# Optimization experiments

Hardware: AMD Instinct MI355X
Metric: run time of the kernel (lower is better)

Reference implementation:

```python
import jax, jax.numpy as jnp
import numpy as np

RES = (256, 256, 256)
CH = 16
RR = 8  # ceil(log2(256))
N_PTS = 262144


def grid_sample_2d(plane, gx, gy):
    """Bilinear grid_sample, align_corners=True.
    plane: (C, H, W); gx in [-1,1] indexes W, gy indexes H. Returns (N, C)."""
    C, H, W = plane.shape
    ix = (gx + 1.0) * 0.5 * (W - 1)
    iy = (gy + 1.0) * 0.5 * (H - 1)
    x0f = jnp.floor(ix)
    y0f = jnp.floor(iy)
    wx = ix - x0f
    wy = iy - y0f
    x0 = jnp.clip(x0f.astype(jnp.int32), 0, W - 1)
    x1 = jnp.clip(x0 + 1, 0, W - 1)
    y0 = jnp.clip(y0f.astype(jnp.int32), 0, H - 1)
    y1 = jnp.clip(y0 + 1, 0, H - 1)
    v00 = plane[:, y0, x0]  # (C, N)
    v01 = plane[:, y0, x1]
    v10 = plane[:, y1, x0]
    v11 = plane[:, y1, x1]
    out = (v00 * (1 - wx) * (1 - wy) + v01 * wx * (1 - wy)
           + v10 * (1 - wx) * wy + v11 * wx * wy)
    return out.T  # (N, C)


def integrate(P, coords):
    """P: (N, 2*CH, RR) with real part channels [:CH], imag [CH:].
    coords: (N,) in [-1,1]. Fourier-basis numerical integration (real part)."""
    c = (coords + 1.0) * 0.5 * (2 ** RR - 1)  # (N,)
    coef = jnp.concatenate([jnp.zeros((1,), jnp.float32),
                            2.0 ** jnp.arange(RR - 1, dtype=jnp.float32)]) / (2 ** RR)
    theta = 2.0 * jnp.pi * c[:, None] * coef  # (N, RR)
    # Re(exp(i*theta) . P_complex) = cos.Re(P) - sin.Im(P)
    re = jnp.einsum('nr,ncr->nc', jnp.cos(theta), P[:, :CH, :])
    im = jnp.einsum('nr,ncr->nc', jnp.sin(theta), P[:, CH:, :])
    return re - im  # (N, CH)


def setup_inputs() -> dict:
    key = jax.random.key(0)
    k0, k1, k2, k3 = jax.random.split(key, 4)
    inputs = jax.random.uniform(k0, (N_PTS, 3), dtype=jnp.float32,
                                minval=-1.0, maxval=1.0)
    C = 2 * RR * CH
    Pu = 0.001 * jax.random.normal(k1, (1, C, RES[1], RES[2]), dtype=jnp.float32)
    Pv = 0.001 * jax.random.normal(k2, (1, C, RES[0], RES[2]), dtype=jnp.float32)
    Pw = 0.001 * jax.random.normal(k3, (1, C, RES[0], RES[1]), dtype=jnp.float32)
    return {"inputs": inputs, "Pu": Pu, "Pv": Pv, "Pw": Pw}


def reference(inputs, Pu, Pv, Pw):
    c0, c1, c2 = inputs[:, 0], inputs[:, 1], inputs[:, 2]
    # grid last-dim (x,y): x indexes width (last plane axis), y the height.
    su = grid_sample_2d(Pu[0], c1, c2).reshape(-1, 2 * CH, RR)
    sv = grid_sample_2d(Pv[0], c0, c2).reshape(-1, 2 * CH, RR)
    sw = grid_sample_2d(Pw[0], c0, c1).reshape(-1, 2 * CH, RR)
    return integrate(su, c0) + integrate(sv, c1) + integrate(sw, c2)  # (N, CH)
```

## Files before the change

kernel.cpp:

```cpp
#include <hip/hip_runtime.h>
#include <hip/hip_fp16.h>
#include <math.h>

#define NPTS 262144
#define PLANE_ELEMS 16777216u

typedef __attribute__((ext_vector_type(4))) float f4;
typedef __attribute__((ext_vector_type(4))) unsigned int u4;

#define OFF_SORTED   (3ull * PLANE_ELEMS * 2ull)
#define OFF_PARTIAL  (OFF_SORTED + (size_t)3 * NPTS * 16)
#define OFF_HIST     (OFF_PARTIAL + (size_t)3 * NPTS * 16 * 2)
#define WS_NEED      (OFF_HIST + (size_t)3 * 65536 * 4)

__device__ __forceinline__ void plane_xy(int p, float c0, float c1, float c2,
                                         float& gx, float& gy, float& ax) {
  if (p == 0)      { gx = c1; gy = c2; ax = c0; }
  else if (p == 1) { gx = c0; gy = c2; ax = c1; }
  else             { gx = c0; gy = c1; ax = c2; }
}

__device__ __forceinline__ int cell_of(float g) {
  float i = (g + 1.f) * 0.5f * 255.f;
  int x0 = (int)floorf(i);
  return x0 < 0 ? 0 : (x0 > 255 ? 255 : x0);
}

__global__ __launch_bounds__(256) void PREFFFT_trans_k(
    const float* __restrict__ Pu, const float* __restrict__ Pv,
    const float* __restrict__ Pw, __half* __restrict__ dst0) {
  __shared__ unsigned tile[128 * 36];
  const float* src = blockIdx.z == 0 ? Pu : (blockIdx.z == 1 ? Pv : Pw);
  __half* dst = dst0 + (size_t)blockIdx.z * PLANE_ELEMS;
  const unsigned hw0 = blockIdx.x * 128u;
  const unsigned c0 = blockIdx.y * 64u;
  const int tid = threadIdx.x;

  f4 va[4], vb[4];
#pragma unroll
  for (int j = 0; j < 4; ++j) {
    int idx = j * 256 + tid;
    int rp = idx >> 5;
    int q = idx & 31;
    const float* base = src + (size_t)(c0 + 2 * rp) * 65536u + hw0 + 4 * q;
    va[j] = *(const f4*)(base);
    vb[j] = *(const f4*)(base + 65536);
  }
#pragma unroll
  for (int j = 0; j < 4; ++j) {
    int idx = j * 256 + tid;
    int rp = idx >> 5;
    int q = idx & 31;
#pragma unroll
    for (int k = 0; k < 4; ++k) {
      int hw = 4 * q + k;
      __half2 h = __floats2half2_rn(va[j][k], vb[j][k]);
      tile[hw * 36 + (rp ^ (hw >> 3))] = *(unsigned*)&h;
    }
  }
  __syncthreads();
  int seg = tid & 7;
#pragma unroll
  for (int jj = 0; jj < 4; ++jj) {
    int hw = jj * 32 + (tid >> 3);
    int s = hw >> 3;
    u4 v = *(const u4*)(tile + hw * 36 + 4 * ((seg ^ (s >> 2)) & 7));
    u4 o;
    switch (s & 3) {
      case 0: o = v; break;
      case 1: o = u4{v.y, v.x, v.w, v.z}; break;
      case 2: o = u4{v.z, v.w, v.x, v.y}; break;
      default: o = u4{v.w, v.z, v.y, v.x}; break;
    }
    *(u4*)((char*)dst + ((size_t)(hw0 + hw) * 256u + c0) * 2u + seg * 16u) = o;
  }
}

__global__ __launch_bounds__(256) void PREFFFT_hist_k(
    const float* __restrict__ inputs, unsigned* __restrict__ hist) {
  int n = blockIdx.x * 256 + threadIdx.x;
  if (n >= NPTS) return;
  float c0 = inputs[n * 3 + 0], c1 = inputs[n * 3 + 1], c2 = inputs[n * 3 + 2];
#pragma unroll
  for (int p = 0; p < 3; ++p) {
    float gx, gy, ax;
    plane_xy(p, c0, c1, c2, gx, gy, ax);
    int key = (cell_of(gy) << 8) | cell_of(gx);
    atomicAdd(&hist[p * 65536 + key], 1u);
  }
}

__global__ __launch_bounds__(1024) void PREFFFT_scan_k(unsigned* __restrict__ hist) {
  __shared__ unsigned part[1024];
  unsigned* h = hist + (size_t)blockIdx.x * 65536;
  int t = threadIdx.x;
  unsigned s = 0;
#pragma unroll 8
  for (int i = 0; i < 64; ++i) s += h[t * 64 + i];
  part[t] = s;
  __syncthreads();
  for (int off = 1; off < 1024; off <<= 1) {
    unsigned v = (t >= off) ? part[t - off] : 0u;
    __syncthreads();
    part[t] += v;
    __syncthreads();
  }
  unsigned run = (t == 0) ? 0u : part[t - 1];
#pragma unroll 8
  for (int i = 0; i < 64; ++i) {
    unsigned c = h[t * 64 + i];
    h[t * 64 + i] = run;
    run += c;
  }
}

__global__ __launch_bounds__(256) void PREFFFT_scat_k(
    const float* __restrict__ inputs, unsigned* __restrict__ hist,
    float4* __restrict__ sortedC) {
  int n = blockIdx.x * 256 + threadIdx.x;
  if (n >= NPTS) return;
  float c0 = inputs[n * 3 + 0], c1 = inputs[n * 3 + 1], c2 = inputs[n * 3 + 2];
#pragma unroll
  for (int p = 0; p < 3; ++p) {
    float gx, gy, ax;
    plane_xy(p, c0, c1, c2, gx, gy, ax);
    int key = (cell_of(gy) << 8) | cell_of(gx);
    unsigned pos = atomicAdd(&hist[p * 65536 + key], 1u);
    sortedC[(size_t)p * NPTS + pos] =
        make_float4(c0, c1, c2, __uint_as_float((unsigned)n));
  }
}

__global__ __launch_bounds__(256) void PREFFFT_samp_k(
    const float4* __restrict__ sortedC, const __half* __restrict__ T,
    __half* __restrict__ partial) {
  int p = blockIdx.y;
  int bx = blockIdx.x;
  int lbx = (bx & 7) * 1024 + (bx >> 3);
  int slot = lbx * 32 + ((int)threadIdx.x >> 3);
  int t = threadIdx.x & 7;

  float4 sc = sortedC[(size_t)p * NPTS + slot];
  unsigned n = __float_as_uint(sc.w);
  float gx, gy, ax;
  plane_xy(p, sc.x, sc.y, sc.z, gx, gy, ax);

  float ix = (gx + 1.f) * 0.5f * 255.f;
  float iy = (gy + 1.f) * 0.5f * 255.f;
  float x0f = floorf(ix), y0f = floorf(iy);
  float wx = ix - x0f, wy = iy - y0f;
  int x0 = (int)x0f; x0 = x0 < 0 ? 0 : (x0 > 255 ? 255 : x0);
  int y0 = (int)y0f; y0 = y0 < 0 ? 0 : (y0 > 255 ? 255 : y0);
  int x1 = x0 + 1 > 255 ? 255 : x0 + 1;
  int y1 = y0 + 1 > 255 ? 255 : y0 + 1;
  float w00 = (1.f - wx) * (1.f - wy);
  float w01 = wx * (1.f - wy);
  float w10 = (1.f - wx) * wy;
  float w11 = wx * wy;

  const __half* __restrict__ P = T + (size_t)p * PLANE_ELEMS;
  int r00 = (y0 * 256 + x0) * 256, r01 = (y0 * 256 + x1) * 256;
  int r10 = (y1 * 256 + x0) * 256, r11 = (y1 * 256 + x1) * 256;
  int ore = t * 16;
  int oim = 128 + t * 16;

  f4 a0 = *(const f4*)(P + r00 + ore),     a1 = *(const f4*)(P + r00 + ore + 8);
  f4 a2 = *(const f4*)(P + r00 + oim),     a3 = *(const f4*)(P + r00 + oim + 8);
  f4 b0 = *(const f4*)(P + r01 + ore),     b1 = *(const f4*)(P + r01 + ore + 8);
  f4 b2 = *(const f4*)(P + r01 + oim),     b3 = *(const f4*)(P + r01 + oim + 8);
  f4 c0v = *(const f4*)(P + r10 + ore),    c1v = *(const f4*)(P + r10 + ore + 8);
  f4 c2v = *(const f4*)(P + r10 + oim),    c3v = *(const f4*)(P + r10 + oim + 8);
  f4 d0 = *(const f4*)(P + r11 + ore),     d1 = *(const f4*)(P + r11 + ore + 8);
  f4 d2 = *(const f4*)(P + r11 + oim),     d3 = *(const f4*)(P + r11 + oim + 8);

  __half2 hw00 = __float2half2_rn(w00), hw01 = __float2half2_rn(w01);
  __half2 hw10 = __float2half2_rn(w10), hw11 = __float2half2_rn(w11);

  __half2 bre[8], bim[8];
#pragma unroll
  for (int q = 0; q < 4; ++q) {
    __half2 v;
    v = __hmul2(((const __half2*)&a0)[q], hw00);
    v = __hfma2(((const __half2*)&b0)[q],  hw01, v);
    v = __hfma2(((const __half2*)&c0v)[q], hw10, v);
    bre[q] = __hfma2(((const __half2*)&d0)[q], hw11, v);

    v = __hmul2(((const __half2*)&a1)[q], hw00);
    v = __hfma2(((const __half2*)&b1)[q],  hw01, v);
    v = __hfma2(((const __half2*)&c1v)[q], hw10, v);
    bre[q + 4] = __hfma2(((const __half2*)&d1)[q], hw11, v);

    v = __hmul2(((const __half2*)&a2)[q], hw00);
    v = __hfma2(((const __half2*)&b2)[q],  hw01, v);
    v = __hfma2(((const __half2*)&c2v)[q], hw10, v);
    bim[q] = __hfma2(((const __half2*)&d2)[q], hw11, v);

    v = __hmul2(((const __half2*)&a3)[q], hw00);
    v = __hfma2(((const __half2*)&b3)[q],  hw01, v);
    v = __hfma2(((const __half2*)&c3v)[q], hw10, v);
    bim[q + 4] = __hfma2(((const __half2*)&d3)[q], hw11, v);
  }

  float fre[16], fim[16];
#pragma unroll
  for (int q = 0; q < 8; ++q) {
    float2 vr = __half22float2(bre[q]);
    float2 vi = __half22float2(bim[q]);
    fre[2 * q] = vr.x; fre[2 * q + 1] = vr.y;
    fim[2 * q] = vi.x; fim[2 * q + 1] = vi.y;
  }

  float cs = (ax + 1.f) * 0.5f * 255.f;
  float th = 6.283185307179586f * cs * (1.f / 256.f);
  float s, c;
  __sincosf(th, &s, &c);
  float aR0 = fre[0], aR1 = fre[8];
  float aI0 = 0.f,    aI1 = 0.f;
#pragma unroll
  for (int r = 1; r < 8; ++r) {
    aR0 += fre[r] * c;     aR1 += fre[8 + r] * c;
    aI0 += fim[r] * s;     aI1 += fim[8 + r] * s;
    if (r < 7) {
      float c2 = c + c;
      float cn = c2 * c - 1.f;
      s = c2 * s;
      c = cn;
    }
  }

  *(__half2*)(partial + ((size_t)p * NPTS + n) * 16 + 2 * t) =
      __floats2half2_rn(aR0 - aI0, aR1 - aI1);
}

__global__ __launch_bounds__(256) void PREFFFT_red_k(
    const __half* __restrict__ part, float* __restrict__ out) {
  size_t i = (size_t)blockIdx.x * 256 + threadIdx.x;
  const size_t PS = (size_t)NPTS * 16;
  union H8 { u4 v; __half2 h[4]; };
  H8 a, b, c;
  a.v = *(const u4*)(part + i * 8);
  b.v = *(const u4*)(part + PS + i * 8);
  c.v = *(const u4*)(part + 2 * PS + i * 8);
  f4 o0, o1;
#pragma unroll
  for (int k = 0; k < 4; ++k) {
    float2 fa = __half22float2(a.h[k]);
    float2 fb = __half22float2(b.h[k]);
    float2 fc = __half22float2(c.h[k]);
    float lo = fa.x + fb.x + fc.x;
    float hi = fa.y + fb.y + fc.y;
    if (k < 2) { o0[2 * k] = lo; o0[2 * k + 1] = hi; }
    else       { o1[2 * (k - 2)] = lo; o1[2 * (k - 2) + 1] = hi; }
  }
  ((f4*)out)[i * 2] = o0;
  ((f4*)out)[i * 2 + 1] = o1;
}

__global__ __launch_bounds__(256) void PREFFFT_fallback_k(
    const float* __restrict__ inputs, const float* __restrict__ Tu,
    const float* __restrict__ Tv, const float* __restrict__ Tw,
    float* __restrict__ out) {
  int gtid = blockIdx.x * 256 + threadIdx.x;
  int n = gtid >> 5;
  int t = threadIdx.x & 31;
  const bool is_re = t < 16;
  float c0 = inputs[n * 3 + 0], c1 = inputs[n * 3 + 1], c2 = inputs[n * 3 + 2];
  const float* PL[3] = {Tu, Tv, Tw};
  float acc = 0.f;
#pragma unroll
  for (int p = 0; p < 3; ++p) {
    float gx, gy, ax;
    plane_xy(p, c0, c1, c2, gx, gy, ax);
    float ix = (gx + 1.f) * 0.5f * 255.f;
    float iy = (gy + 1.f) * 0.5f * 255.f;
    float x0f = floorf(ix), y0f = floorf(iy);
    float wx = ix - x0f, wy = iy - y0f;
    int x0 = (int)x0f; x0 = x0 < 0 ? 0 : (x0 > 255 ? 255 : x0);
    int y0 = (int)y0f; y0 = y0 < 0 ? 0 : (y0 > 255 ? 255 : y0);
    int x1 = x0 + 1 > 255 ? 255 : x0 + 1;
    int y1 = y0 + 1 > 255 ? 255 : y0 + 1;
    float w00 = (1.f - wx) * (1.f - wy), w01 = wx * (1.f - wy);
    float w10 = (1.f - wx) * wy, w11 = wx * wy;
    int i00 = y0 * 256 + x0, i01 = y0 * 256 + x1;
    int i10 = y1 * 256 + x0, i11 = y1 * 256 + x1;
    float b[8];
#pragma unroll
    for (int j = 0; j < 8; ++j) {
      const float* base = PL[p] + (size_t)(t * 8 + j) * 65536u;
      b[j] = w00 * base[i00] + w01 * base[i01] + w10 * base[i10] + w11 * base[i11];
    }
    float csv = (ax + 1.f) * 0.5f * 255.f;
    float theta1 = 6.283185307179586f * csv * (1.f / 256.f);
    float partial = is_re ? b[0] : 0.f;
#pragma unroll
    for (int r = 1; r < 8; ++r) {
      float thr = theta1 * (float)(1 << (r - 1));
      float s, c;
      __sincosf(thr, &s, &c);
      partial += b[r] * (is_re ? c : s);
    }
    float other = __shfl_xor(partial, 16);
    acc += partial - other;
  }
  if (is_re) out[n * 16 + t] = acc;
}

extern "C" void kernel_launch(void* const* d_in, const int* in_sizes, int n_in,
                              void* d_out, int out_size, void* d_ws, size_t ws_size,
                              hipStream_t stream) {
  const float* inputs = (const float*)d_in[0];
  const float* Pu = (const float*)d_in[1];
  const float* Pv = (const float*)d_in[2];
  const float* Pw = (const float*)d_in[3];
  float* out = (float*)d_out;

  if (ws_size >= WS_NEED) {
    char* ws = (char*)d_ws;
    __half*   T       = (__half*)ws;
    float4*   sortedC = (float4*)(ws + OFF_SORTED);
    __half*   partial = (__half*)(ws + OFF_PARTIAL);
    unsigned* hist    = (unsigned*)(ws + OFF_HIST);

    {
      dim3 tg(512, 4, 3);
      PREFFFT_trans_k<<<tg, 256, 0, stream>>>(Pu, Pv, Pw, T);
    }
    hipMemsetAsync(hist, 0, (size_t)3 * 65536 * 4, stream);
    PREFFFT_hist_k<<<NPTS / 256, 256, 0, stream>>>(inputs, hist);
    PREFFFT_scan_k<<<3, 1024, 0, stream>>>(hist);
    PREFFFT_scat_k<<<NPTS / 256, 256, 0, stream>>>(inputs, hist, sortedC);
    {
      dim3 tg(NPTS / 32, 3);
      PREFFFT_samp_k<<<tg, 256, 0, stream>>>(sortedC, T, partial);
    }
    PREFFFT_red_k<<<2048, 256, 0, stream>>>(partial, out);
  } else {
    PREFFFT_fallback_k<<<NPTS / 8, 256, 0, stream>>>(inputs, Pu, Pv, Pw, out);
  }
}
```

Measured before the change: 235.4 us.

## Software-pipeline plane transpose over four tiles with nontemporal loads

The transpose kernel now handles four 128-column tiles per block, loading the next tile into registers while the current one is written through shared memory, with an added barrier between tiles. Loads use nontemporal hints, and the grid shrinks to match. The scatter kernel also stores the already-permuted per-plane coordinates so the sampling kernel skips the plane-selection logic. The intent is to hide global load latency in the bandwidth-bound fp32-to-fp16 transpose, at the cost of more registers and fewer blocks in flight.

```diff
diff --git a/kernel.cpp b/kernel.cpp
--- a/kernel.cpp
+++ b/kernel.cpp
@@ -26,26 +26,23 @@
   return x0 < 0 ? 0 : (x0 > 255 ? 255 : x0);
 }
 
-__global__ __launch_bounds__(256) void PREFFFT_trans_k(
-    const float* __restrict__ Pu, const float* __restrict__ Pv,
-    const float* __restrict__ Pw, __half* __restrict__ dst0) {
-  __shared__ unsigned tile[128 * 36];
-  const float* src = blockIdx.z == 0 ? Pu : (blockIdx.z == 1 ? Pv : Pw);
-  __half* dst = dst0 + (size_t)blockIdx.z * PLANE_ELEMS;
-  const unsigned hw0 = blockIdx.x * 128u;
-  const unsigned c0 = blockIdx.y * 64u;
-  const int tid = threadIdx.x;
-
-  f4 va[4], vb[4];
+__device__ __forceinline__ void trans_load(const float* __restrict__ src,
+                                           unsigned c0, unsigned hw0, int tid,
+                                           f4 (&va)[4], f4 (&vb)[4]) {
 #pragma unroll
   for (int j = 0; j < 4; ++j) {
     int idx = j * 256 + tid;
     int rp = idx >> 5;
     int q = idx & 31;
-    const float* base = src + (size_t)(c0 + 2 * rp) * 65536u + hw0 + 4 * q;
-    va[j] = *(const f4*)(base);
-    vb[j] = *(const f4*)(base + 65536);
-  }
+    const f4* base = (const f4*)(src + (size_t)(c0 + 2 * rp) * 65536u + hw0 + 4 * q);
+    va[j] = __builtin_nontemporal_load(base);
+    vb[j] = __builtin_nontemporal_load(base + 16384);
+  }
+}
+
+__device__ __forceinline__ void trans_proc(unsigned* tile, __half* dst,
+                                           unsigned c0, unsigned hw0, int tid,
+                                           f4 (&va)[4], f4 (&vb)[4]) {
 #pragma unroll
   for (int j = 0; j < 4; ++j) {
     int idx = j * 256 + tid;
@@ -74,6 +71,28 @@
     }
     *(u4*)((char*)dst + ((size_t)(hw0 + hw) * 256u + c0) * 2u + seg * 16u) = o;
   }
+  __syncthreads();
+}
+
+__global__ __launch_bounds__(256) void PREFFFT_trans_k(
+    const float* __restrict__ Pu, const float* __restrict__ Pv,
+    const float* __restrict__ Pw, __half* __restrict__ dst0) {
+  __shared__ unsigned tile[128 * 36];
+  const float* src = blockIdx.z == 0 ? Pu : (blockIdx.z == 1 ? Pv : Pw);
+  __half* dst = dst0 + (size_t)blockIdx.z * PLANE_ELEMS;
+  const unsigned hwbase = blockIdx.x * 512u;
+  const unsigned c0 = blockIdx.y * 64u;
+  const int tid = threadIdx.x;
+
+  f4 vaA[4], vbA[4], vaB[4], vbB[4];
+  trans_load(src, c0, hwbase, tid, vaA, vbA);
+  trans_load(src, c0, hwbase + 128u, tid, vaB, vbB);
+  trans_proc(tile, dst, c0, hwbase, tid, vaA, vbA);
+  trans_load(src, c0, hwbase + 256u, tid, vaA, vbA);
+  trans_proc(tile, dst, c0, hwbase + 128u, tid, vaB, vbB);
+  trans_load(src, c0, hwbase + 384u, tid, vaB, vbB);
+  trans_proc(tile, dst, c0, hwbase + 256u, tid, vaA, vbA);
+  trans_proc(tile, dst, c0, hwbase + 384u, tid, vaB, vbB);
 }
 
 __global__ __launch_bounds__(256) void PREFFFT_hist_k(
@@ -127,7 +146,7 @@
     int key = (cell_of(gy) << 8) | cell_of(gx);
     unsigned pos = atomicAdd(&hist[p * 65536 + key], 1u);
     sortedC[(size_t)p * NPTS + pos] =
-        make_float4(c0, c1, c2, __uint_as_float((unsigned)n));
+        make_float4(gx, gy, ax, __uint_as_float((unsigned)n));
   }
 }
 
@@ -142,8 +161,7 @@
 
   float4 sc = sortedC[(size_t)p * NPTS + slot];
   unsigned n = __float_as_uint(sc.w);
-  float gx, gy, ax;
-  plane_xy(p, sc.x, sc.y, sc.z, gx, gy, ax);
+  float gx = sc.x, gy = sc.y, ax = sc.z;
 
   float ix = (gx + 1.f) * 0.5f * 255.f;
   float iy = (gy + 1.f) * 0.5f * 255.f;
@@ -322,7 +340,7 @@
     unsigned* hist    = (unsigned*)(ws + OFF_HIST);
 
     {
-      dim3 tg(512, 4, 3);
+      dim3 tg(128, 4, 3);
       PREFFFT_trans_k<<<tg, 256, 0, stream>>>(Pu, Pv, Pw, T);
     }
     hipMemsetAsync(hist, 0, (size_t)3 * 65536 * 4, stream);
```

Measured after the change: 228.3 us. 1.03x faster.
